# Kernel optimization log

Measured on AMD Instinct MI355X. Metric: run time of the kernel, lower is better.

## Reference

```python
import jax, jax.numpy as jnp
import numpy as np

SIGMA = 0.1  # kernel-point influence radius (KPConv linear correlation)


def setup_inputs() -> dict:
    key = jax.random.key(0)
    k1, k2, k3, k4, k5 = jax.random.split(key, 5)
    N, K, KP, CIN, COUT = 65536, 32, 15, 64, 128
    pos = jax.random.uniform(k1, (N, 3), dtype=jnp.float32)
    feats = jax.random.normal(k2, (N, CIN), dtype=jnp.float32)
    kernel_points = jax.random.normal(k3, (KP, 3), dtype=jnp.float32) * 0.05
    weights = jax.random.normal(k4, (KP, CIN, COUT), dtype=jnp.float32) / np.sqrt(KP * CIN)
    neighbors = jax.random.randint(k5, (N, K), 0, N, dtype=jnp.int64)
    return {"pos": pos, "feats": feats, "kernel_points": kernel_points,
            "weights": weights, "neighbors": neighbors}


def reference(pos, feats, kernel_points, weights, neighbors):
    # pos: [N,3], feats: [N,Cin], kernel_points: [Kp,3],
    # weights: [Kp,Cin,Cout], neighbors: [N,K] int
    neigh_pos = pos[neighbors]                      # [N,K,3] irregular gather
    rel = neigh_pos - pos[:, None, :]               # [N,K,3]
    # distance from each relative neighbor offset to each kernel point
    d = rel[:, :, None, :] - kernel_points[None, None, :, :]   # [N,K,Kp,3]
    dist = jnp.sqrt(jnp.sum(d * d, axis=-1))        # [N,K,Kp]
    infl = jnp.maximum(0.0, 1.0 - dist / SIGMA)     # linear correlation
    neigh_feat = feats[neighbors]                   # [N,K,Cin] irregular gather
    # per-kernel-point weighted neighbor aggregation, then projection
    weighted = jnp.einsum('njk,njc->nkc', infl, neigh_feat)    # [N,Kp,Cin]
    out = jnp.einsum('nkc,kcd->nd', weighted, weights)         # [N,Cout]
    return out
```

## Files before the change

### kernel.cpp

```cpp
#include <hip/hip_runtime.h>

#define NPTS  65536
#define KNB   32
#define KPn   15
#define CIN   64
#define COUT  128
#define MPTS  16
#define THREADS 512
#define WSTRIDE 968
#define BCAP  48
#define RCAP  96
#define NTILE 8
#define KSTEPS 30
#define WELEMS (NTILE * KSTEPS * 64 * 8)

typedef __attribute__((ext_vector_type(8))) short short8;
typedef __attribute__((ext_vector_type(4))) float f32x4;

__device__ __forceinline__ unsigned int f2bf(float f) {
    union { float f; unsigned int i; } v; v.f = f;
    return (v.i + 0x7fffu + ((v.i >> 16) & 1u)) >> 16;
}

__global__ void wtrans_kernel(const float* __restrict__ w,
                              const float* __restrict__ kpts,
                              unsigned short* __restrict__ wTf,
                              float4* __restrict__ kpq_out) {
    const int d = blockIdx.x * 256 + threadIdx.x;
    if (d < WELEMS) {
        const int j    = d & 7;
        const int lane = (d >> 3) & 63;
        const int ks   = (d >> 9) % KSTEPS;
        const int t    = d / (KSTEPS * 512);
        const int f    = ks * 32 + (lane >> 4) * 8 + j;
        const int cg   = f / 120;
        const int rem  = f - cg * 120;
        const int orig = (rem >> 3) * 64 + cg * 8 + (rem & 7);
        const int n    = t * 16 + (lane & 15);
        wTf[d] = (unsigned short)f2bf(w[(size_t)orig * COUT + n]);
    }
    if (blockIdx.x == 0 && threadIdx.x < 16) {
        const int k = threadIdx.x;
        if (k < KPn) {
            const float x = kpts[k * 3 + 0];
            const float y = kpts[k * 3 + 1];
            const float z = kpts[k * 3 + 2];
            kpq_out[k] = make_float4(x, y, z, x * x + y * y + z * z);
        } else {
            float mx = 0.f;
            for (int i = 0; i < KPn; ++i) {
                const float x = kpts[i * 3 + 0];
                const float y = kpts[i * 3 + 1];
                const float z = kpts[i * 3 + 2];
                mx = fmaxf(mx, x * x + y * y + z * z);
            }
            const float R = 0.1f + sqrtf(mx);
            kpq_out[15] = make_float4(R * R, 0.f, 0.f, 0.f);
        }
    }
}

__global__ __launch_bounds__(THREADS, 8) void kpconv_kernel(
    const float* __restrict__ pos,
    const float* __restrict__ feats,
    const unsigned short* __restrict__ wTf,
    const float4* __restrict__ kpq_in,
    const int*   __restrict__ neighbors,
    float*       __restrict__ out)
{
    __shared__ unsigned short wl[MPTS * WSTRIDE];
    __shared__ unsigned int  bpk[MPTS][BCAP];
    __shared__ int    bcnt[MPTS];
    __shared__ float  cposf[MPTS * 3];
    __shared__ float4 kpq[KPn];
    __shared__ float  rlx[RCAP], rly[RCAP], rlz[RCAP], rld[RCAP];
    __shared__ unsigned int rsl[RCAP];
    __shared__ int    nact;
    __shared__ float  R2s;

    const int tid = threadIdx.x;
    const int n0  = blockIdx.x * MPTS;

    if (tid < KPn) kpq[tid] = kpq_in[tid];
    if (tid == KPn) R2s = kpq_in[15].x;
    if (tid < MPTS) bcnt[tid] = 0;
    if (tid == THREADS - 1) nact = 0;
    if (tid < MPTS * 3) cposf[tid] = pos[(size_t)n0 * 3 + tid];
    __syncthreads();

    {
        const float R2 = R2s;
        const int s  = tid;
        const int p  = s >> 5;
        const int nb = neighbors[(size_t)n0 * KNB + s];
        const float rx = pos[(size_t)nb * 3 + 0] - cposf[p * 3 + 0];
        const float ry = pos[(size_t)nb * 3 + 1] - cposf[p * 3 + 1];
        const float rz = pos[(size_t)nb * 3 + 2] - cposf[p * 3 + 2];
        const float d2r = rx * rx + ry * ry + rz * rz;
        if (d2r < R2) {
            const int idx = atomicAdd(&nact, 1);
            if (idx < RCAP) {
                rlx[idx] = rx; rly[idx] = ry; rlz[idx] = rz; rld[idx] = d2r;
                rsl[idx] = ((unsigned int)p << 16) | (unsigned int)nb;
            }
        }
    }
    __syncthreads();

    {
        const int E = min(nact, RCAP);
        for (int u = tid; u < E * 16; u += THREADS) {
            const int e = u >> 4;
            const int k = u & 15;
            if (k < KPn) {
                const float4 kp  = kpq[k];
                const float  d2r = rld[e];
                const float dot = rlx[e] * kp.x + rly[e] * kp.y + rlz[e] * kp.z;
                if (dot > 0.5f * (d2r - 0.01f + kp.w)) {
                    const float d2 = fmaxf(d2r - 2.f * dot + kp.w, 0.f);
                    const float w  = 1.0f - 10.0f * sqrtf(d2);
                    const unsigned int wq = (unsigned int)(w * 4095.0f + 0.5f);
                    const unsigned int sl = rsl[e];
                    const int p = (int)(sl >> 16);
                    const int idx = atomicAdd(&bcnt[p], 1);
                    if (idx < BCAP)
                        bpk[p][idx] = ((sl & 0xFFFFu) << 16) |
                                      ((unsigned int)k << 12) | wq;
                }
            }
        }
    }
    __syncthreads();

    #pragma unroll
    for (int it = 0; it < 4; ++it) {
        const int wi = tid + it * THREADS;
        const int cg = wi & 7;
        const int k  = (wi >> 3) & 15;
        const int p  = wi >> 7;
        if (k < KPn) {
            float a0=0.f,a1=0.f,a2=0.f,a3=0.f,a4=0.f,a5=0.f,a6=0.f,a7=0.f;
            const int cnt = min(bcnt[p], BCAP);
            for (int e = 0; e < cnt; ++e) {
                const unsigned int id = bpk[p][e];
                if (((id >> 12) & 15u) == (unsigned int)k) {
                    const float wv = (float)(id & 4095u) * (1.0f / 4095.0f);
                    const float* fr = feats + (size_t)(id >> 16) * CIN + cg * 8;
                    const float4 f0 = *(const float4*)fr;
                    const float4 f1 = *(const float4*)(fr + 4);
                    a0 += wv * f0.x; a1 += wv * f0.y; a2 += wv * f0.z; a3 += wv * f0.w;
                    a4 += wv * f1.x; a5 += wv * f1.y; a6 += wv * f1.z; a7 += wv * f1.w;
                }
            }
            uint4 u;
            u.x = f2bf(a0) | (f2bf(a1) << 16);
            u.y = f2bf(a2) | (f2bf(a3) << 16);
            u.z = f2bf(a4) | (f2bf(a5) << 16);
            u.w = f2bf(a6) | (f2bf(a7) << 16);
            *(uint4*)(wl + p * WSTRIDE + cg * 120 + k * 8) = u;
        }
    }
    __syncthreads();

    {
        const int wave = tid >> 6;
        const int lane = tid & 63;
        const int m    = lane & 15;
        const int q    = lane >> 4;

        f32x4 acc = {0.f, 0.f, 0.f, 0.f};
        const unsigned short* ap = wl + m * WSTRIDE + q * 8;
        const short8* bp = (const short8*)wTf + (size_t)wave * KSTEPS * 64 + lane;

        #pragma unroll 5
        for (int ks = 0; ks < KSTEPS; ++ks, ap += 32) {
            const short8 a = *(const short8*)ap;
            const short8 b = bp[ks * 64];
            acc = __builtin_amdgcn_mfma_f32_16x16x32_bf16(a, b, acc, 0, 0, 0);
        }

        const int c = wave * 16 + m;
        #pragma unroll
        for (int r = 0; r < 4; ++r)
            out[(size_t)(n0 + q * 4 + r) * COUT + c] = acc[r];
    }
}

extern "C" void kernel_launch(void* const* d_in, const int* in_sizes, int n_in,
                              void* d_out, int out_size, void* d_ws, size_t ws_size,
                              hipStream_t stream) {
    const float* pos       = (const float*)d_in[0];
    const float* feats     = (const float*)d_in[1];
    const float* kpts      = (const float*)d_in[2];
    const float* weights   = (const float*)d_in[3];
    const int*   neighbors = (const int*)d_in[4];
    float*       out       = (float*)d_out;
    unsigned short* wTf    = (unsigned short*)d_ws;
    float4* kpq            = (float4*)((char*)d_ws + WELEMS * 2);

    wtrans_kernel<<<(WELEMS + 255) / 256, 256, 0, stream>>>(weights, kpts, wTf, kpq);
    kpconv_kernel<<<NPTS / MPTS, THREADS, 0, stream>>>(
        pos, feats, wTf, kpq, neighbors, out);
}
```

Before: 138.3 us.

## Stage active neighbor features in LDS as bf16 and hoist neighbor position loads

After: 138.9 us. Within noise of the previous version (+0.4%).

```diff
diff --git a/kernel.cpp b/kernel.cpp
--- a/kernel.cpp
+++ b/kernel.cpp
@@ -20,6 +20,12 @@
 __device__ __forceinline__ unsigned int f2bf(float f) {
     union { float f; unsigned int i; } v; v.f = f;
     return (v.i + 0x7fffu + ((v.i >> 16) & 1u)) >> 16;
+}
+__device__ __forceinline__ float bflo(unsigned int u) {
+    union { unsigned int i; float f; } v; v.i = u << 16; return v.f;
+}
+__device__ __forceinline__ float bfhi(unsigned int u) {
+    union { unsigned int i; float f; } v; v.i = u & 0xFFFF0000u; return v.f;
 }
 
 __global__ void wtrans_kernel(const float* __restrict__ w,
@@ -68,7 +74,8 @@
     const int*   __restrict__ neighbors,
     float*       __restrict__ out)
 {
-    __shared__ unsigned short wl[MPTS * WSTRIDE];
+    __shared__ __align__(16) unsigned short wl[MPTS * WSTRIDE];
+    __shared__ __align__(16) unsigned short sfeat[RCAP * CIN];
     __shared__ unsigned int  bpk[MPTS][BCAP];
     __shared__ int    bcnt[MPTS];
     __shared__ float  cposf[MPTS * 3];
@@ -76,56 +83,68 @@
     __shared__ float  rlx[RCAP], rly[RCAP], rlz[RCAP], rld[RCAP];
     __shared__ unsigned int rsl[RCAP];
     __shared__ int    nact;
-    __shared__ float  R2s;
 
     const int tid = threadIdx.x;
     const int n0  = blockIdx.x * MPTS;
 
+    const int   p0  = tid >> 5;
+    const int   nb0 = neighbors[(size_t)n0 * KNB + tid];
+    const float qx  = pos[(size_t)nb0 * 3 + 0];
+    const float qy  = pos[(size_t)nb0 * 3 + 1];
+    const float qz  = pos[(size_t)nb0 * 3 + 2];
+    const float R2  = kpq_in[15].x;
+
     if (tid < KPn) kpq[tid] = kpq_in[tid];
-    if (tid == KPn) R2s = kpq_in[15].x;
     if (tid < MPTS) bcnt[tid] = 0;
-    if (tid == THREADS - 1) nact = 0;
+    if (tid == 0) nact = 0;
     if (tid < MPTS * 3) cposf[tid] = pos[(size_t)n0 * 3 + tid];
     __syncthreads();
 
     {
-        const float R2 = R2s;
-        const int s  = tid;
-        const int p  = s >> 5;
-        const int nb = neighbors[(size_t)n0 * KNB + s];
-        const float rx = pos[(size_t)nb * 3 + 0] - cposf[p * 3 + 0];
-        const float ry = pos[(size_t)nb * 3 + 1] - cposf[p * 3 + 1];
-        const float rz = pos[(size_t)nb * 3 + 2] - cposf[p * 3 + 2];
+        const float rx = qx - cposf[p0 * 3 + 0];
+        const float ry = qy - cposf[p0 * 3 + 1];
+        const float rz = qz - cposf[p0 * 3 + 2];
         const float d2r = rx * rx + ry * ry + rz * rz;
         if (d2r < R2) {
             const int idx = atomicAdd(&nact, 1);
             if (idx < RCAP) {
                 rlx[idx] = rx; rly[idx] = ry; rlz[idx] = rz; rld[idx] = d2r;
-                rsl[idx] = ((unsigned int)p << 16) | (unsigned int)nb;
+                rsl[idx] = ((unsigned int)p0 << 16) | (unsigned int)nb0;
             }
         }
     }
     __syncthreads();
 
     {
-        const int E = min(nact, RCAP);
-        for (int u = tid; u < E * 16; u += THREADS) {
-            const int e = u >> 4;
-            const int k = u & 15;
-            if (k < KPn) {
-                const float4 kp  = kpq[k];
-                const float  d2r = rld[e];
-                const float dot = rlx[e] * kp.x + rly[e] * kp.y + rlz[e] * kp.z;
-                if (dot > 0.5f * (d2r - 0.01f + kp.w)) {
-                    const float d2 = fmaxf(d2r - 2.f * dot + kp.w, 0.f);
-                    const float w  = 1.0f - 10.0f * sqrtf(d2);
-                    const unsigned int wq = (unsigned int)(w * 4095.0f + 0.5f);
-                    const unsigned int sl = rsl[e];
-                    const int p = (int)(sl >> 16);
-                    const int idx = atomicAdd(&bcnt[p], 1);
-                    if (idx < BCAP)
-                        bpk[p][idx] = ((sl & 0xFFFFu) << 16) |
-                                      ((unsigned int)k << 12) | wq;
+        const int E      = min(nact, RCAP);
+        const int staged = E * 16;
+        for (int u = tid; u < staged * 2; u += THREADS) {
+            if (u < staged) {
+                const int e = u >> 4;
+                const int c = u & 15;
+                const int nb = (int)(rsl[e] & 0xFFFFu);
+                const float4 f = *(const float4*)(feats + (size_t)nb * CIN + c * 4);
+                const unsigned int lo = f2bf(f.x) | (f2bf(f.y) << 16);
+                const unsigned int hi = f2bf(f.z) | (f2bf(f.w) << 16);
+                *(uint2*)(sfeat + e * CIN + c * 4) = make_uint2(lo, hi);
+            } else {
+                const int v = u - staged;
+                const int e = v >> 4;
+                const int k = v & 15;
+                if (k < KPn) {
+                    const float4 kp  = kpq[k];
+                    const float  d2r = rld[e];
+                    const float dot = rlx[e] * kp.x + rly[e] * kp.y + rlz[e] * kp.z;
+                    if (dot > 0.5f * (d2r - 0.01f + kp.w)) {
+                        const float d2 = fmaxf(d2r - 2.f * dot + kp.w, 0.f);
+                        const float w  = 1.0f - 10.0f * sqrtf(d2);
+                        const unsigned int wq = (unsigned int)(w * 4095.0f + 0.5f);
+                        const int p = (int)(rsl[e] >> 16);
+                        const int idx = atomicAdd(&bcnt[p], 1);
+                        if (idx < BCAP)
+                            bpk[p][idx] = ((unsigned int)e << 16) |
+                                          ((unsigned int)k << 12) | wq;
+                    }
                 }
             }
         }
@@ -145,11 +164,11 @@
                 const unsigned int id = bpk[p][e];
                 if (((id >> 12) & 15u) == (unsigned int)k) {
                     const float wv = (float)(id & 4095u) * (1.0f / 4095.0f);
-                    const float* fr = feats + (size_t)(id >> 16) * CIN + cg * 8;
-                    const float4 f0 = *(const float4*)fr;
-                    const float4 f1 = *(const float4*)(fr + 4);
-                    a0 += wv * f0.x; a1 += wv * f0.y; a2 += wv * f0.z; a3 += wv * f0.w;
-                    a4 += wv * f1.x; a5 += wv * f1.y; a6 += wv * f1.z; a7 += wv * f1.w;
+                    const uint4 vf = *(const uint4*)(sfeat + (id >> 16) * CIN + cg * 8);
+                    a0 += wv * bflo(vf.x); a1 += wv * bfhi(vf.x);
+                    a2 += wv * bflo(vf.y); a3 += wv * bfhi(vf.y);
+                    a4 += wv * bflo(vf.z); a5 += wv * bfhi(vf.z);
+                    a6 += wv * bflo(vf.w); a7 += wv * bfhi(vf.w);
                 }
             }
             uint4 u;
```

## Replace shared-memory binning with wave-level ballot and readlane neighbor aggregation

Applied to the files above, without the earlier changes.

Measured after the change: 144.4 us. 4.5% more time.

```diff
diff --git a/kernel.cpp b/kernel.cpp
--- a/kernel.cpp
+++ b/kernel.cpp
@@ -8,8 +8,6 @@
 #define MPTS  16
 #define THREADS 512
 #define WSTRIDE 968
-#define BCAP  48
-#define RCAP  96
 #define NTILE 8
 #define KSTEPS 30
 #define WELEMS (NTILE * KSTEPS * 64 * 8)
@@ -20,6 +18,11 @@
 __device__ __forceinline__ unsigned int f2bf(float f) {
     union { float f; unsigned int i; } v; v.f = f;
     return (v.i + 0x7fffu + ((v.i >> 16) & 1u)) >> 16;
+}
+__device__ __forceinline__ float rlanef(float v, int l) {
+    union { float f; int i; } u; u.f = v;
+    u.i = __builtin_amdgcn_readlane(u.i, l);
+    return u.f;
 }
 
 __global__ void wtrans_kernel(const float* __restrict__ w,
@@ -60,6 +63,30 @@
     }
 }
 
+#define PROC_HALF(MSK, ACC)                                                   \
+    {                                                                         \
+        unsigned long long msk_ = (MSK);                                      \
+        while (msk_) {                                                        \
+            const int j_ = (int)__builtin_ctzll(msk_);                        \
+            msk_ &= msk_ - 1;                                                 \
+            const int   nbs_ = __builtin_amdgcn_readlane(nbv, j_);            \
+            const float rxs_ = rlanef(rx, j_);                                \
+            const float rys_ = rlanef(ry, j_);                                \
+            const float rzs_ = rlanef(rz, j_);                                \
+            const float d2s_ = rlanef(d2r, j_);                               \
+            const float f_   = feats[(size_t)nbs_ * CIN + lane];              \
+            _Pragma("unroll")                                                 \
+            for (int k = 0; k < KPn; ++k) {                                   \
+                const float  dot = rxs_ * kpx[k] + rys_ * kpy[k] + rzs_ * kpz[k]; \
+                if (dot > 0.5f * (d2s_ - 0.01f + kpw[k])) {                   \
+                    const float dd = fmaxf(d2s_ - 2.f * dot + kpw[k], 0.f);   \
+                    const float w_ = 1.0f - 10.0f * sqrtf(dd);                \
+                    ACC[k] += w_ * f_;                                        \
+                }                                                             \
+            }                                                                 \
+        }                                                                     \
+    }
+
 __global__ __launch_bounds__(THREADS, 8) void kpconv_kernel(
     const float* __restrict__ pos,
     const float* __restrict__ feats,
@@ -68,121 +95,84 @@
     const int*   __restrict__ neighbors,
     float*       __restrict__ out)
 {
-    __shared__ unsigned short wl[MPTS * WSTRIDE];
-    __shared__ unsigned int  bpk[MPTS][BCAP];
-    __shared__ int    bcnt[MPTS];
-    __shared__ float  cposf[MPTS * 3];
-    __shared__ float4 kpq[KPn];
-    __shared__ float  rlx[RCAP], rly[RCAP], rlz[RCAP], rld[RCAP];
-    __shared__ unsigned int rsl[RCAP];
-    __shared__ int    nact;
-    __shared__ float  R2s;
+    __shared__ __align__(16) unsigned short wl[MPTS * WSTRIDE];
 
-    const int tid = threadIdx.x;
-    const int n0  = blockIdx.x * MPTS;
+    const int tid  = threadIdx.x;
+    const int n0   = blockIdx.x * MPTS;
+    const int lane = tid & 63;
+    const int wv   = tid >> 6;
+    const int m    = lane & 15;
+    const int q    = lane >> 4;
 
-    if (tid < KPn) kpq[tid] = kpq_in[tid];
-    if (tid == KPn) R2s = kpq_in[15].x;
-    if (tid < MPTS) bcnt[tid] = 0;
-    if (tid == THREADS - 1) nact = 0;
-    if (tid < MPTS * 3) cposf[tid] = pos[(size_t)n0 * 3 + tid];
-    __syncthreads();
+    const int nbv = neighbors[(size_t)n0 * KNB + tid];
+    const float px = pos[(size_t)nbv * 3 + 0];
+    const float py = pos[(size_t)nbv * 3 + 1];
+    const float pz = pos[(size_t)nbv * 3 + 2];
+
+    float kpx[KPn], kpy[KPn], kpz[KPn], kpw[KPn];
+    #pragma unroll
+    for (int k = 0; k < KPn; ++k) {
+        const float4 kp = kpq_in[k];
+        kpx[k] = kp.x; kpy[k] = kp.y; kpz[k] = kp.z; kpw[k] = kp.w;
+    }
+    const float R2 = kpq_in[15].x;
+
+    const int nAu = __builtin_amdgcn_readfirstlane(n0 + wv * 2);
+    const float cxA = pos[(size_t)nAu * 3 + 0];
+    const float cyA = pos[(size_t)nAu * 3 + 1];
+    const float czA = pos[(size_t)nAu * 3 + 2];
+    const float cxB = pos[(size_t)(nAu + 1) * 3 + 0];
+    const float cyB = pos[(size_t)(nAu + 1) * 3 + 1];
+    const float czB = pos[(size_t)(nAu + 1) * 3 + 2];
+
+    const bool isA = (lane < 32);
+    const float rx = px - (isA ? cxA : cxB);
+    const float ry = py - (isA ? cyA : cyB);
+    const float rz = pz - (isA ? czA : czB);
+    const float d2r = rx * rx + ry * ry + rz * rz;
+
+    const unsigned long long bal = __ballot(d2r < R2);
+
+    float accA[KPn], accB[KPn];
+    #pragma unroll
+    for (int k = 0; k < KPn; ++k) { accA[k] = 0.f; accB[k] = 0.f; }
+
+    PROC_HALF(bal & 0x00000000ffffffffull, accA);
+    PROC_HALF(bal & 0xffffffff00000000ull, accB);
 
     {
-        const float R2 = R2s;
-        const int s  = tid;
-        const int p  = s >> 5;
-        const int nb = neighbors[(size_t)n0 * KNB + s];
-        const float rx = pos[(size_t)nb * 3 + 0] - cposf[p * 3 + 0];
-        const float ry = pos[(size_t)nb * 3 + 1] - cposf[p * 3 + 1];
-        const float rz = pos[(size_t)nb * 3 + 2] - cposf[p * 3 + 2];
-        const float d2r = rx * rx + ry * ry + rz * rz;
-        if (d2r < R2) {
-            const int idx = atomicAdd(&nact, 1);
-            if (idx < RCAP) {
-                rlx[idx] = rx; rly[idx] = ry; rlz[idx] = rz; rld[idx] = d2r;
-                rsl[idx] = ((unsigned int)p << 16) | (unsigned int)nb;
-            }
+        const int cg = lane >> 3, j = lane & 7;
+        unsigned short* wpA = wl + (wv * 2 + 0) * WSTRIDE + cg * 120 + j;
+        unsigned short* wpB = wl + (wv * 2 + 1) * WSTRIDE + cg * 120 + j;
+        #pragma unroll
+        for (int k = 0; k < KPn; ++k) {
+            wpA[k * 8] = (unsigned short)f2bf(accA[k]);
+            wpB[k * 8] = (unsigned short)f2bf(accB[k]);
         }
     }
     __syncthreads();
 
     {
-        const int E = min(nact, RCAP);
-        for (int u = tid; u < E * 16; u += THREADS) {
-            const int e = u >> 4;
-            const int k = u & 15;
-            if (k < KPn) {
-                const float4 kp  = kpq[k];
-                const float  d2r = rld[e];
-                const float dot = rlx[e] * kp.x + rly[e] * kp.y + rlz[e] * kp.z;
-                if (dot > 0.5f * (d2r - 0.01f + kp.w)) {
-                    const float d2 = fmaxf(d2r - 2.f * dot + kp.w, 0.f);
-                    const float w  = 1.0f - 10.0f * sqrtf(d2);
-                    const unsigned int wq = (unsigned int)(w * 4095.0f + 0.5f);
-                    const unsigned int sl = rsl[e];
-                    const int p = (int)(sl >> 16);
-                    const int idx = atomicAdd(&bcnt[p], 1);
-                    if (idx < BCAP)
-                        bpk[p][idx] = ((sl & 0xFFFFu) << 16) |
-                                      ((unsigned int)k << 12) | wq;
-                }
-            }
+        f32x4 o0 = {0.f, 0.f, 0.f, 0.f};
+        f32x4 o1 = {0.f, 0.f, 0.f, 0.f};
+        const unsigned short* ap = wl + m * WSTRIDE + q * 8;
+        const short8* bp = (const short8*)wTf + (size_t)wv * KSTEPS * 64 + lane;
+
+        #pragma unroll 3
+        for (int ks = 0; ks < KSTEPS; ks += 2) {
+            const short8 a0 = *(const short8*)(ap + ks * 32);
+            const short8 b0 = bp[ks * 64];
+            o0 = __builtin_amdgcn_mfma_f32_16x16x32_bf16(a0, b0, o0, 0, 0, 0);
+            const short8 a1 = *(const short8*)(ap + (ks + 1) * 32);
+            const short8 b1 = bp[(ks + 1) * 64];
+            o1 = __builtin_amdgcn_mfma_f32_16x16x32_bf16(a1, b1, o1, 0, 0, 0);
         }
-    }
-    __syncthreads();
+        o0 = o0 + o1;
 
-    #pragma unroll
-    for (int it = 0; it < 4; ++it) {
-        const int wi = tid + it * THREADS;
-        const int cg = wi & 7;
-        const int k  = (wi >> 3) & 15;
-        const int p  = wi >> 7;
-        if (k < KPn) {
-            float a0=0.f,a1=0.f,a2=0.f,a3=0.f,a4=0.f,a5=0.f,a6=0.f,a7=0.f;
-            const int cnt = min(bcnt[p], BCAP);
-            for (int e = 0; e < cnt; ++e) {
-                const unsigned int id = bpk[p][e];
-                if (((id >> 12) & 15u) == (unsigned int)k) {
-                    const float wv = (float)(id & 4095u) * (1.0f / 4095.0f);
-                    const float* fr = feats + (size_t)(id >> 16) * CIN + cg * 8;
-                    const float4 f0 = *(const float4*)fr;
-                    const float4 f1 = *(const float4*)(fr + 4);
-                    a0 += wv * f0.x; a1 += wv * f0.y; a2 += wv * f0.z; a3 += wv * f0.w;
-                    a4 += wv * f1.x; a5 += wv * f1.y; a6 += wv * f1.z; a7 += wv * f1.w;
-                }
-            }
-            uint4 u;
-            u.x = f2bf(a0) | (f2bf(a1) << 16);
-            u.y = f2bf(a2) | (f2bf(a3) << 16);
-            u.z = f2bf(a4) | (f2bf(a5) << 16);
-            u.w = f2bf(a6) | (f2bf(a7) << 16);
-            *(uint4*)(wl + p * WSTRIDE + cg * 120 + k * 8) = u;
-        }
-    }
-    __syncthreads();
-
-    {
-        const int wave = tid >> 6;
-        const int lane = tid & 63;
-        const int m    = lane & 15;
-        const int q    = lane >> 4;
-
-        f32x4 acc = {0.f, 0.f, 0.f, 0.f};
-        const unsigned short* ap = wl + m * WSTRIDE + q * 8;
-        const short8* bp = (const short8*)wTf + (size_t)wave * KSTEPS * 64 + lane;
-
-        #pragma unroll 5
-        for (int ks = 0; ks < KSTEPS; ++ks, ap += 32) {
-            const short8 a = *(const short8*)ap;
-            const short8 b = bp[ks * 64];
-            acc = __builtin_amdgcn_mfma_f32_16x16x32_bf16(a, b, acc, 0, 0, 0);
-        }
-
-        const int c = wave * 16 + m;
+        const int c = wv * 16 + m;
         #pragma unroll
         for (int r = 0; r < 4; ++r)
-            out[(size_t)(n0 + q * 4 + r) * COUT + c] = acc[r];
+            out[(size_t)(n0 + q * 4 + r) * COUT + c] = o0[r];
     }
 }
 
```
